# Optimization experiments

Hardware: AMD Instinct MI355X
Metric: run time of the kernel (lower is better)

Reference implementation:

```python
import jax, jax.numpy as jnp
import numpy as np

EPS = 1e-5

def _bn(x, g, b):
    # training-mode BatchNorm1d over the batch axis (axis 0), biased variance
    m = jnp.mean(x, axis=0)
    v = jnp.var(x, axis=0)
    return g * (x - m) / jnp.sqrt(v + EPS) + b

def _mlp(x, w1, b1, g1, be1, w2, b2, g2, be2, w3, b3):
    # Linear -> BN -> ReLU -> Linear -> BN -> ReLU -> Linear
    x = jax.nn.relu(_bn(x @ w1.T + b1, g1, be1))
    x = jax.nn.relu(_bn(x @ w2.T + b2, g2, be2))
    return x @ w3.T + b3

def setup_inputs() -> dict:
    key = jax.random.key(0)
    ks = jax.random.split(key, 10)
    B, S, D = 256, 512, 128
    w = lambda k: jax.random.normal(k, (D, D), jnp.float32) * 0.05
    return {
        "s": jax.random.normal(ks[0], (B, S, D), jnp.float32),
        "c": jax.random.normal(ks[1], (B, D), jnp.float32),
        "s_w1": w(ks[2]), "s_b1": jnp.zeros((D,), jnp.float32),
        "s_g1": jnp.ones((D,), jnp.float32), "s_be1": jnp.zeros((D,), jnp.float32),
        "s_w2": w(ks[3]), "s_b2": jnp.zeros((D,), jnp.float32),
        "s_g2": jnp.ones((D,), jnp.float32), "s_be2": jnp.zeros((D,), jnp.float32),
        "s_w3": w(ks[4]), "s_b3": jnp.zeros((D,), jnp.float32),
        "c_w1": w(ks[5]), "c_b1": jnp.zeros((D,), jnp.float32),
        "c_g1": jnp.ones((D,), jnp.float32), "c_be1": jnp.zeros((D,), jnp.float32),
        "c_w2": w(ks[6]), "c_b2": jnp.zeros((D,), jnp.float32),
        "c_g2": jnp.ones((D,), jnp.float32), "c_be2": jnp.zeros((D,), jnp.float32),
        "c_w3": w(ks[7]), "c_b3": jnp.zeros((D,), jnp.float32),
    }

def reference(s, c,
              s_w1, s_b1, s_g1, s_be1, s_w2, s_b2, s_g2, s_be2, s_w3, s_b3,
              c_w1, c_b1, c_g1, c_be1, c_w2, c_b2, c_g2, c_be2, c_w3, c_b3):
    # c_mlp: [B, D] -> [B, D] (BN over batch)
    c_out = _mlp(c, c_w1, c_b1, c_g1, c_be1, c_w2, c_b2, c_g2, c_be2, c_w3, c_b3)
    # s_mlp applied per sequence slice; BN stats over batch axis 0 only
    # (matches the torch loop where each s[:, i, :] gets its own BN stats).
    # s: [B, S, D]; _bn with axis=0 gives per-(slice, feature) stats.
    s_h = _mlp(s, s_w1, s_b1, s_g1, s_be1, s_w2, s_b2, s_g2, s_be2, s_w3, s_b3)
    s_out = s_h * c_out[:, None, :]          # context gate, [B, S, D]
    aggregated_c = jnp.max(s_out, axis=1)    # pooling == 'max', [B, D]
    return (s_out, aggregated_c)
```

## Files before the change

### kernel.cpp

```cpp
#include <hip/hip_runtime.h>
#include <hip/hip_bf16.h>
#include <math.h>

#define BATCH 256
#define SEQ   512
#define DIM   128
#define LDSK  136
#define LDSF  132

typedef __attribute__((ext_vector_type(8))) __bf16  bf16x8;
typedef __attribute__((ext_vector_type(4))) __bf16  bf16x4;
typedef __attribute__((ext_vector_type(4))) float   f32x4;

template<int RT>
__device__ __forceinline__ void matmul_layer(
    const __bf16* __restrict__ Xa, const __bf16* __restrict__ wg,
    const float* __restrict__ bias, f32x4 (&acc)[RT][8], int wave, int m, int q)
{
  const int rowbase = wave * RT * 16;
#pragma unroll
  for (int ct = 0; ct < 8; ++ct) {
    const float b = bias[ct * 16 + m];
    const f32x4 bv = {b, b, b, b};
#pragma unroll
    for (int rt = 0; rt < RT; ++rt) acc[rt][ct] = bv;
  }
#pragma unroll
  for (int ks = 0; ks < 4; ++ks) {
    const int k0 = ks * 32 + q * 8;
    bf16x8 a[RT], bw[8];
#pragma unroll
    for (int rt = 0; rt < RT; ++rt)
      a[rt] = *(const bf16x8*)(Xa + (rowbase + rt * 16 + m) * LDSK + k0);
#pragma unroll
    for (int ct = 0; ct < 8; ++ct)
      bw[ct] = *(const bf16x8*)(wg + (ct * 16 + m) * DIM + k0);
#pragma unroll
    for (int rt = 0; rt < RT; ++rt)
#pragma unroll
      for (int ct = 0; ct < 8; ++ct)
        acc[rt][ct] = __builtin_amdgcn_mfma_f32_16x16x32_bf16(a[rt], bw[ct], acc[rt][ct], 0, 0, 0);
  }
}

template<int RT>
__device__ __forceinline__ void stats_accum(
    const f32x4 (&acc)[RT][8], float* sumA, float* sqA, int m, int q)
{
#pragma unroll
  for (int ct = 0; ct < 8; ++ct) {
    float s = 0.f, ss = 0.f;
#pragma unroll
    for (int rt = 0; rt < RT; ++rt)
#pragma unroll
      for (int r = 0; r < 4; ++r) { const float v = acc[rt][ct][r]; s += v; ss += v * v; }
    s  += __shfl_xor(s, 16, 64);  s  += __shfl_xor(s, 32, 64);
    ss += __shfl_xor(ss, 16, 64); ss += __shfl_xor(ss, 32, 64);
    if (q == 0) { atomicAdd(&sumA[ct * 16 + m], s); atomicAdd(&sqA[ct * 16 + m], ss); }
  }
}

__device__ __forceinline__ void bn_coefs(int tid, const float* __restrict__ g,
    const float* __restrict__ be, float* sumA, float* sqA, float* cA, float* cC)
{
  if (tid < DIM) {
    const float mean = sumA[tid] * (1.0f / BATCH);
    const float var  = sqA[tid]  * (1.0f / BATCH) - mean * mean;
    const float rstd = rsqrtf(var + 1e-5f);
    const float a = g[tid] * rstd;
    cA[tid] = a;
    cC[tid] = be[tid] - a * mean;
    sumA[tid] = 0.f; sqA[tid] = 0.f;
  }
}

template<int RT>
__device__ __forceinline__ void bn_relu_store(
    const f32x4 (&acc)[RT][8], __bf16* Xa, const float* cA, const float* cC,
    int wave, int m, int q)
{
  const int rowbase = wave * RT * 16;
#pragma unroll
  for (int ct = 0; ct < 8; ++ct) {
    const int n = ct * 16 + m;
    const float a = cA[n], c = cC[n];
#pragma unroll
    for (int rt = 0; rt < RT; ++rt)
#pragma unroll
      for (int r = 0; r < 4; ++r) {
        const float y = fmaxf(0.f, a * acc[rt][ct][r] + c);
        const int row = rowbase + rt * 16 + q * 4 + r;
        Xa[row * LDSK + n] = (__bf16)y;
      }
  }
}

template<int NW, bool GATE>
__global__ __launch_bounds__(NW * 64, NW / 2)
void mlp_kernel(const float* __restrict__ xin, long xrow_stride,
                const __bf16* __restrict__ w1, const __bf16* __restrict__ w2,
                const __bf16* __restrict__ w3,
                const float* __restrict__ b1, const float* __restrict__ g1, const float* __restrict__ be1,
                const float* __restrict__ b2, const float* __restrict__ g2, const float* __restrict__ be2,
                const float* __restrict__ b3,
                const float* __restrict__ gate,
                float* __restrict__ out)
{
  const int tid  = threadIdx.x;
  constexpr int NT = NW * 64;
  constexpr int RT = 16 / NW;
  const int wave = tid >> 6, lane = tid & 63;
  const int m = lane & 15, q = lane >> 4;
  const int slice = GATE ? blockIdx.x : 0;
  const float* x0 = GATE ? (xin + (long)slice * DIM) : xin;

  __shared__ __align__(16) char XaRaw[BATCH * LDSK * 2];
  __bf16* Xa = (__bf16*)XaRaw;
  __shared__ float sumA[DIM], sqA[DIM], cA[DIM], cC[DIM];

  for (int t = tid; t < DIM; t += NT) { sumA[t] = 0.f; sqA[t] = 0.f; }

  {
    const int rpi = NT / 32;
    const int r0  = tid >> 5;
    const int c4  = (tid & 31) * 4;
#pragma unroll
    for (int it = 0; it < BATCH / rpi; ++it) {
      const int r = it * rpi + r0;
      const float4 v = *(const float4*)(x0 + (long)r * xrow_stride + c4);
      bf16x4 h = { (__bf16)v.x, (__bf16)v.y, (__bf16)v.z, (__bf16)v.w };
      *(bf16x4*)(Xa + r * LDSK + c4) = h;
    }
  }
  __syncthreads();

  f32x4 acc[RT][8];

  matmul_layer<RT>(Xa, w1, b1, acc, wave, m, q);
  stats_accum<RT>(acc, sumA, sqA, m, q);
  __syncthreads();
  bn_coefs(tid, g1, be1, sumA, sqA, cA, cC);
  __syncthreads();
  bn_relu_store<RT>(acc, Xa, cA, cC, wave, m, q);
  __syncthreads();

  matmul_layer<RT>(Xa, w2, b2, acc, wave, m, q);
  stats_accum<RT>(acc, sumA, sqA, m, q);
  __syncthreads();
  bn_coefs(tid, g2, be2, sumA, sqA, cA, cC);
  __syncthreads();
  bn_relu_store<RT>(acc, Xa, cA, cC, wave, m, q);
  __syncthreads();

  matmul_layer<RT>(Xa, w3, b3, acc, wave, m, q);

  if constexpr (GATE) {
    float* Xf = (float*)XaRaw;
    const int c4 = (tid & 31) * 4;
    const int r0 = tid >> 5;
    __syncthreads();
#pragma unroll
    for (int rt = 0; rt < RT; ++rt) {
#pragma unroll
      for (int ct = 0; ct < 8; ++ct)
#pragma unroll
        for (int r = 0; r < 4; ++r)
          Xf[(wave * 16 + q * 4 + r) * LDSF + ct * 16 + m] = acc[rt][ct][r];
      __syncthreads();
#pragma unroll
      for (int it = 0; it < 8; ++it) {
        const int crow = it * 16 + r0;
        const int grow = (crow >> 4) * 32 + rt * 16 + (crow & 15);
        float4 y = *(const float4*)(Xf + crow * LDSF + c4);
        const float4 gv = *(const float4*)(gate + grow * DIM + c4);
        y.x *= gv.x; y.y *= gv.y; y.z *= gv.z; y.w *= gv.w;
        *(float4*)(out + ((long)grow * SEQ + slice) * DIM + c4) = y;
      }
      if (rt + 1 < RT) __syncthreads();
    }
  } else {
    const int rowbase = wave * RT * 16;
#pragma unroll
    for (int ct = 0; ct < 8; ++ct) {
      const int col = ct * 16 + m;
#pragma unroll
      for (int rt = 0; rt < RT; ++rt) {
#pragma unroll
        for (int r = 0; r < 4; ++r) {
          const int row = rowbase + rt * 16 + q * 4 + r;
          out[row * DIM + col] = acc[rt][ct][r];
        }
      }
    }
  }
}

__global__ void prep_kernel(const float* __restrict__ w0, const float* __restrict__ w1,
                            const float* __restrict__ w2, const float* __restrict__ w3,
                            const float* __restrict__ w4, const float* __restrict__ w5,
                            __bf16* __restrict__ dst)
{
  const int idx = blockIdx.x * blockDim.x + threadIdx.x;
  const int mi  = idx >> 12;
  const int j   = (idx & 4095) * 4;
  const float* srcs[6] = {w0, w1, w2, w3, w4, w5};
  const float4 v = *(const float4*)(srcs[mi] + j);
  bf16x4 h = { (__bf16)v.x, (__bf16)v.y, (__bf16)v.z, (__bf16)v.w };
  *(bf16x4*)(dst + mi * 16384 + j) = h;
}

__global__ __launch_bounds__(1024) void maxpool_kernel(
    const float* __restrict__ sout, float* __restrict__ agg)
{
  __shared__ float4 red[1024];
  const int b = blockIdx.x;
  const int t = threadIdx.x;
  const int c4 = (t & 31) * 4, rg = t >> 5;
  const float* p = sout + (long)b * SEQ * DIM + c4;
  float4 mx = {-INFINITY, -INFINITY, -INFINITY, -INFINITY};
#pragma unroll 4
  for (int i = rg; i < SEQ; i += 32) {
    const float4 v = *(const float4*)(p + (long)i * DIM);
    mx.x = fmaxf(mx.x, v.x); mx.y = fmaxf(mx.y, v.y);
    mx.z = fmaxf(mx.z, v.z); mx.w = fmaxf(mx.w, v.w);
  }
  red[t] = mx;
  __syncthreads();
  if (t < 32) {
    float4 a = red[t];
#pragma unroll
    for (int k = 1; k < 32; ++k) {
      const float4 v = red[t + 32 * k];
      a.x = fmaxf(a.x, v.x); a.y = fmaxf(a.y, v.y);
      a.z = fmaxf(a.z, v.z); a.w = fmaxf(a.w, v.w);
    }
    *(float4*)(agg + b * DIM + c4) = a;
  }
}

extern "C" void kernel_launch(void* const* d_in, const int* in_sizes, int n_in,
                              void* d_out, int out_size, void* d_ws, size_t ws_size,
                              hipStream_t stream)
{
  const float* s     = (const float*)d_in[0];
  const float* c     = (const float*)d_in[1];
  const float* s_w1  = (const float*)d_in[2];
  const float* s_b1  = (const float*)d_in[3];
  const float* s_g1  = (const float*)d_in[4];
  const float* s_be1 = (const float*)d_in[5];
  const float* s_w2  = (const float*)d_in[6];
  const float* s_b2  = (const float*)d_in[7];
  const float* s_g2  = (const float*)d_in[8];
  const float* s_be2 = (const float*)d_in[9];
  const float* s_w3  = (const float*)d_in[10];
  const float* s_b3  = (const float*)d_in[11];
  const float* c_w1  = (const float*)d_in[12];
  const float* c_b1  = (const float*)d_in[13];
  const float* c_g1  = (const float*)d_in[14];
  const float* c_be1 = (const float*)d_in[15];
  const float* c_w2  = (const float*)d_in[16];
  const float* c_b2  = (const float*)d_in[17];
  const float* c_g2  = (const float*)d_in[18];
  const float* c_be2 = (const float*)d_in[19];
  const float* c_w3  = (const float*)d_in[20];
  const float* c_b3  = (const float*)d_in[21];

  float* out   = (float*)d_out;
  float* c_out = (float*)d_ws;
  __bf16* wbf  = (__bf16*)((char*)d_ws + (size_t)BATCH * DIM * sizeof(float));

  prep_kernel<<<96, 256, 0, stream>>>(s_w1, s_w2, s_w3, c_w1, c_w2, c_w3, wbf);

  mlp_kernel<8, false><<<1, 512, 0, stream>>>(
      c, (long)DIM,
      wbf + 3 * 16384, wbf + 4 * 16384, wbf + 5 * 16384,
      c_b1, c_g1, c_be1, c_b2, c_g2, c_be2, c_b3,
      nullptr, c_out);

  mlp_kernel<8, true><<<SEQ, 512, 0, stream>>>(
      s, (long)SEQ * DIM,
      wbf, wbf + 16384, wbf + 2 * 16384,
      s_b1, s_g1, s_be1, s_b2, s_g2, s_be2, s_b3,
      c_out, out);

  maxpool_kernel<<<BATCH, 1024, 0, stream>>>(out, out + (long)BATCH * SEQ * DIM);
}
```

Before: 269.2 us.

## Compute BN coefficients per wave and drop block barriers between MLP layers

Each wave now computes the BatchNorm scale and shift itself from the shared sum and square-sum buffers, instead of one thread group writing coefficients between extra barriers. Separate stat buffers per layer, plus the fact that each wave only reads back its own rows, let two barriers per layer be removed. Weight fragments are loaded in two groups of four to lower register pressure, and partial unroll pragmas are added. The launch bound now asks for 4 blocks per CU, and the context MLP runs with 16 waves. The tighter launch bound may cap VGPRs enough to force spills, and LDS use likely prevents reaching that occupancy anyway.

```diff
diff --git a/kernel.cpp b/kernel.cpp
--- a/kernel.cpp
+++ b/kernel.cpp
@@ -28,24 +28,29 @@
 #pragma unroll
   for (int ks = 0; ks < 4; ++ks) {
     const int k0 = ks * 32 + q * 8;
-    bf16x8 a[RT], bw[8];
+    bf16x8 a[RT];
 #pragma unroll
     for (int rt = 0; rt < RT; ++rt)
       a[rt] = *(const bf16x8*)(Xa + (rowbase + rt * 16 + m) * LDSK + k0);
 #pragma unroll
-    for (int ct = 0; ct < 8; ++ct)
-      bw[ct] = *(const bf16x8*)(wg + (ct * 16 + m) * DIM + k0);
-#pragma unroll
-    for (int rt = 0; rt < RT; ++rt)
-#pragma unroll
-      for (int ct = 0; ct < 8; ++ct)
-        acc[rt][ct] = __builtin_amdgcn_mfma_f32_16x16x32_bf16(a[rt], bw[ct], acc[rt][ct], 0, 0, 0);
+    for (int cg = 0; cg < 2; ++cg) {
+      bf16x8 bw[4];
+#pragma unroll
+      for (int cj = 0; cj < 4; ++cj)
+        bw[cj] = *(const bf16x8*)(wg + ((cg * 4 + cj) * 16 + m) * DIM + k0);
+#pragma unroll
+      for (int rt = 0; rt < RT; ++rt)
+#pragma unroll
+        for (int cj = 0; cj < 4; ++cj)
+          acc[rt][cg * 4 + cj] =
+              __builtin_amdgcn_mfma_f32_16x16x32_bf16(a[rt], bw[cj], acc[rt][cg * 4 + cj], 0, 0, 0);
+    }
   }
 }
 
 template<int RT>
 __device__ __forceinline__ void stats_accum(
-    const f32x4 (&acc)[RT][8], float* sumA, float* sqA, int m, int q)
+    const f32x4 (&acc)[RT][8], float* sumL, float* sqL, int m, int q)
 {
 #pragma unroll
   for (int ct = 0; ct < 8; ++ct) {
@@ -56,34 +61,24 @@
       for (int r = 0; r < 4; ++r) { const float v = acc[rt][ct][r]; s += v; ss += v * v; }
     s  += __shfl_xor(s, 16, 64);  s  += __shfl_xor(s, 32, 64);
     ss += __shfl_xor(ss, 16, 64); ss += __shfl_xor(ss, 32, 64);
-    if (q == 0) { atomicAdd(&sumA[ct * 16 + m], s); atomicAdd(&sqA[ct * 16 + m], ss); }
-  }
-}
-
-__device__ __forceinline__ void bn_coefs(int tid, const float* __restrict__ g,
-    const float* __restrict__ be, float* sumA, float* sqA, float* cA, float* cC)
-{
-  if (tid < DIM) {
-    const float mean = sumA[tid] * (1.0f / BATCH);
-    const float var  = sqA[tid]  * (1.0f / BATCH) - mean * mean;
-    const float rstd = rsqrtf(var + 1e-5f);
-    const float a = g[tid] * rstd;
-    cA[tid] = a;
-    cC[tid] = be[tid] - a * mean;
-    sumA[tid] = 0.f; sqA[tid] = 0.f;
+    if (q == 0) { atomicAdd(&sumL[ct * 16 + m], s); atomicAdd(&sqL[ct * 16 + m], ss); }
   }
 }
 
 template<int RT>
 __device__ __forceinline__ void bn_relu_store(
-    const f32x4 (&acc)[RT][8], __bf16* Xa, const float* cA, const float* cC,
+    const f32x4 (&acc)[RT][8], __bf16* Xa, const float* sumL, const float* sqL,
+    const float* __restrict__ g, const float* __restrict__ be,
     int wave, int m, int q)
 {
   const int rowbase = wave * RT * 16;
 #pragma unroll
   for (int ct = 0; ct < 8; ++ct) {
     const int n = ct * 16 + m;
-    const float a = cA[n], c = cC[n];
+    const float mean = sumL[n] * (1.0f / BATCH);
+    const float var  = sqL[n]  * (1.0f / BATCH) - mean * mean;
+    const float a = g[n] * rsqrtf(var + 1e-5f);
+    const float c = be[n] - a * mean;
 #pragma unroll
     for (int rt = 0; rt < RT; ++rt)
 #pragma unroll
@@ -96,7 +91,7 @@
 }
 
 template<int NW, bool GATE>
-__global__ __launch_bounds__(NW * 64, NW / 2)
+__global__ __launch_bounds__(NW * 64, (NW == 8) ? 4 : 2)
 void mlp_kernel(const float* __restrict__ xin, long xrow_stride,
                 const __bf16* __restrict__ w1, const __bf16* __restrict__ w2,
                 const __bf16* __restrict__ w3,
@@ -116,15 +111,15 @@
 
   __shared__ __align__(16) char XaRaw[BATCH * LDSK * 2];
   __bf16* Xa = (__bf16*)XaRaw;
-  __shared__ float sumA[DIM], sqA[DIM], cA[DIM], cC[DIM];
-
-  for (int t = tid; t < DIM; t += NT) { sumA[t] = 0.f; sqA[t] = 0.f; }
+  __shared__ float sum1[DIM], sq1[DIM], sum2[DIM], sq2[DIM];
+
+  for (int t = tid; t < DIM; t += NT) { sum1[t] = 0.f; sq1[t] = 0.f; sum2[t] = 0.f; sq2[t] = 0.f; }
 
   {
     const int rpi = NT / 32;
     const int r0  = tid >> 5;
     const int c4  = (tid & 31) * 4;
-#pragma unroll
+#pragma unroll 4
     for (int it = 0; it < BATCH / rpi; ++it) {
       const int r = it * rpi + r0;
       const float4 v = *(const float4*)(x0 + (long)r * xrow_stride + c4);
@@ -137,20 +132,14 @@
   f32x4 acc[RT][8];
 
   matmul_layer<RT>(Xa, w1, b1, acc, wave, m, q);
-  stats_accum<RT>(acc, sumA, sqA, m, q);
-  __syncthreads();
-  bn_coefs(tid, g1, be1, sumA, sqA, cA, cC);
-  __syncthreads();
-  bn_relu_store<RT>(acc, Xa, cA, cC, wave, m, q);
-  __syncthreads();
+  stats_accum<RT>(acc, sum1, sq1, m, q);
+  __syncthreads();
+  bn_relu_store<RT>(acc, Xa, sum1, sq1, g1, be1, wave, m, q);
 
   matmul_layer<RT>(Xa, w2, b2, acc, wave, m, q);
-  stats_accum<RT>(acc, sumA, sqA, m, q);
-  __syncthreads();
-  bn_coefs(tid, g2, be2, sumA, sqA, cA, cC);
-  __syncthreads();
-  bn_relu_store<RT>(acc, Xa, cA, cC, wave, m, q);
-  __syncthreads();
+  stats_accum<RT>(acc, sum2, sq2, m, q);
+  __syncthreads();
+  bn_relu_store<RT>(acc, Xa, sum2, sq2, g2, be2, wave, m, q);
 
   matmul_layer<RT>(Xa, w3, b3, acc, wave, m, q);
 
@@ -167,7 +156,7 @@
         for (int r = 0; r < 4; ++r)
           Xf[(wave * 16 + q * 4 + r) * LDSF + ct * 16 + m] = acc[rt][ct][r];
       __syncthreads();
-#pragma unroll
+#pragma unroll 4
       for (int it = 0; it < 8; ++it) {
         const int crow = it * 16 + r0;
         const int grow = (crow >> 4) * 32 + rt * 16 + (crow & 15);
@@ -271,7 +260,7 @@
 
   prep_kernel<<<96, 256, 0, stream>>>(s_w1, s_w2, s_w3, c_w1, c_w2, c_w3, wbf);
 
-  mlp_kernel<8, false><<<1, 512, 0, stream>>>(
+  mlp_kernel<16, false><<<1, 1024, 0, stream>>>(
       c, (long)DIM,
       wbf + 3 * 16384, wbf + 4 * 16384, wbf + 5 * 16384,
       c_b1, c_g1, c_be1, c_b2, c_g2, c_be2, c_b3,
```

Result: slower. 281.6 us (+4.6%).
